# Performance work log

Hardware: AMD Instinct MI355X
Metric: run time of the kernel (lower is better)

## Reference

```python
import jax, jax.numpy as jnp
import numpy as np

SLOPE = 0.15  # LeakyReLU negative slope used throughout the module

def leaky(v):
    return jnp.where(v >= 0, v, SLOPE * v)

def _linear_params(key, fan_in, fan_out):
    kw, kb = jax.random.split(key)
    bound = 1.0 / np.sqrt(fan_in)
    W = jax.random.uniform(kw, (fan_in, fan_out), minval=-bound, maxval=bound, dtype=jnp.float32)
    b = jax.random.uniform(kb, (fan_out,), minval=-bound, maxval=bound, dtype=jnp.float32)
    return W, b

N_NODES = 50000
N_EDGES = 640000
IN_DIM = 128
EDGE_DIM = 64
HID = 128
LAT = 64

def setup_inputs() -> dict:
    key = jax.random.key(0)
    ks = jax.random.split(key, 12)
    x = jax.random.normal(ks[0], (N_NODES, IN_DIM), dtype=jnp.float32)
    edge_index = jax.random.randint(ks[1], (2, N_EDGES), 0, N_NODES, dtype=jnp.int32)
    edge_attr = jax.random.normal(ks[2], (N_EDGES, EDGE_DIM), dtype=jnp.float32)
    # conv1 params
    e1W1, e1b1 = _linear_params(ks[3], EDGE_DIM, HID)
    e1W2, e1b2 = _linear_params(ks[4], HID, HID)
    n1W, n1b = _linear_params(ks[5], IN_DIM + HID, HID)
    # conv2 params
    e2W1, e2b1 = _linear_params(ks[6], EDGE_DIM, HID)
    e2W2, e2b2 = _linear_params(ks[7], HID, HID)
    n2W, n2b = _linear_params(ks[8], HID + HID, HID)
    muW, mub = _linear_params(ks[9], HID, LAT)
    lvW, lvb = _linear_params(ks[10], HID, LAT)
    return {"x": x, "edge_index": edge_index, "edge_attr": edge_attr,
            "e1W1": e1W1, "e1b1": e1b1, "e1W2": e1W2, "e1b2": e1b2, "n1W": n1W, "n1b": n1b,
            "e2W1": e2W1, "e2b1": e2b1, "e2W2": e2W2, "e2b2": e2b2, "n2W": n2W, "n2b": n2b,
            "muW": muW, "mub": mub, "lvW": lvW, "lvb": lvb}

def edge_encoder(x, edge_index, edge_attr, eW1, eb1, eW2, eb2, nW, nb):
    # edge MLP: Linear -> LeakyReLU(0.15) -> Linear
    emb = leaky(edge_attr @ eW1 + eb1) @ eW2 + eb2           # [E, H]
    dst = edge_index[1]                                       # PyG x_i = x[target]
    z = jnp.concatenate([x[dst], emb], axis=1)                # [E, in+H]
    msg = z @ nW + nb                                         # [E, H]
    return jax.ops.segment_sum(msg, dst, num_segments=x.shape[0])  # aggr='add'

def reference(x, edge_index, edge_attr,
              e1W1, e1b1, e1W2, e1b2, n1W, n1b,
              e2W1, e2b1, e2W2, e2b2, n2W, n2b,
              muW, mub, lvW, lvb):
    # Dropout is identity in eval mode.
    h = leaky(edge_encoder(x, edge_index, edge_attr, e1W1, e1b1, e1W2, e1b2, n1W, n1b))
    h = leaky(edge_encoder(h, edge_index, edge_attr, e2W1, e2b1, e2W2, e2b2, n2W, n2b))
    mu = h @ muW + mub
    logvar = h @ lvW + lvb
    return (mu, logvar)
```

## Files before the change

### kernel.cpp

```cpp
#include <hip/hip_runtime.h>

typedef __bf16 bf16x4 __attribute__((ext_vector_type(4)));
typedef __bf16 bf16x8 __attribute__((ext_vector_type(8)));
typedef float  f32x4  __attribute__((ext_vector_type(4)));

constexpr int N_NODES = 50000;
constexpr int N_EDGES = 640000;
constexpr int NTILES  = 98;
constexpr int NB_EDGE = 2500;

__device__ __forceinline__ float leaky(float v) { return v >= 0.f ? v : 0.15f * v; }

__global__ void prep_kernel(
    const float* __restrict__ e1W1, const float* __restrict__ e1b1,
    const float* __restrict__ e1W2, const float* __restrict__ e1b2,
    const float* __restrict__ n1W,  const float* __restrict__ n1b,
    const float* __restrict__ e2W1, const float* __restrict__ e2b1,
    const float* __restrict__ e2W2, const float* __restrict__ e2b2,
    const float* __restrict__ n2W,  const float* __restrict__ n2b,
    const float* __restrict__ muW,  const float* __restrict__ mub,
    const float* __restrict__ lvW,  const float* __restrict__ lvb,
    __bf16* __restrict__ packE, __bf16* __restrict__ packN1,
    __bf16* __restrict__ packN2, __bf16* __restrict__ packH,
    float* __restrict__ ebias, float* __restrict__ c1, float* __restrict__ c2,
    float* __restrict__ hbias)
{
    int bid = blockIdx.x;
    int lane = threadIdx.x;
    int quad = lane >> 4, low = lane & 15;

    if (bid < 32) {
        int ct = bid >> 1, kt = bid & 1;
        for (int j = 0; j < 8; ++j) {
            int k = kt * 32 + quad * 8 + j;
            int n = ct * 16 + low;
            float v = (n < 128) ? e1W1[k * 128 + n] : e2W1[k * 128 + (n - 128)];
            packE[((ct * 2 + kt) * 64 + lane) * 8 + j] = (__bf16)v;
        }
    } else if (bid < 160) {
        bool is1 = bid < 96;
        int tile = bid - (is1 ? 32 : 96);
        const float* nW  = is1 ? n1W  : n2W;
        const float* eW2 = is1 ? e1W2 : e2W2;
        __bf16* dst = is1 ? packN1 : packN2;
        int ct = tile >> 3, kt = tile & 7;
        for (int j = 0; j < 8; ++j) {
            int k = kt * 32 + quad * 8 + j;
            int n = ct * 16 + low;
            float v;
            if (k < 128) {
                v = nW[k * 128 + n];
            } else {
                int i = k - 128;
                float acc = 0.f;
                for (int k2 = 0; k2 < 128; ++k2)
                    acc += eW2[i * 128 + k2] * nW[(128 + k2) * 128 + n];
                v = acc;
            }
            dst[((ct * 8 + kt) * 64 + lane) * 8 + j] = (__bf16)v;
        }
    } else if (bid < 192) {
        int tile = bid - 160;
        int ct = tile >> 2, kt = tile & 3;
        for (int j = 0; j < 8; ++j) {
            int k = kt * 32 + quad * 8 + j;
            int n = ct * 16 + low;
            float v = (n < 64) ? muW[k * 64 + n] : lvW[k * 64 + (n - 64)];
            packH[((ct * 4 + kt) * 64 + lane) * 8 + j] = (__bf16)v;
        }
    } else if (bid == 192 || bid == 193) {
        const float* nW  = (bid == 192) ? n1W  : n2W;
        const float* nb  = (bid == 192) ? n1b  : n2b;
        const float* eb2 = (bid == 192) ? e1b2 : e2b2;
        float* dst = (bid == 192) ? c1 : c2;
        for (int rep = 0; rep < 2; ++rep) {
            int j = lane + rep * 64;
            float acc = nb[j];
            for (int k = 0; k < 128; ++k)
                acc += eb2[k] * nW[(128 + k) * 128 + j];
            dst[j] = acc;
        }
    } else {
        for (int rep = 0; rep < 4; ++rep) {
            int j = lane + rep * 64;
            ebias[j] = (j < 128) ? e1b1[j] : e2b1[j - 128];
        }
        for (int rep = 0; rep < 2; ++rep) {
            int j = lane + rep * 64;
            hbias[j] = (j < 64) ? mub[j] : lvb[j - 64];
        }
    }
}

__global__ void hist_kernel(const int* __restrict__ dstp, int* __restrict__ deg) {
    int e = blockIdx.x * 256 + threadIdx.x;
    if (e < N_EDGES) atomicAdd(&deg[dstp[e]], 1);
}

__global__ void scan_a(const int* __restrict__ deg, int* __restrict__ offs,
                       int* __restrict__ tileSum, float* __restrict__ degf) {
    __shared__ int s[512];
    int t = threadIdx.x, i = blockIdx.x * 512 + t;
    int v = (i < N_NODES) ? deg[i] : 0;
    if (i < N_NODES) degf[i] = (float)v;
    s[t] = v; __syncthreads();
    for (int off = 1; off < 512; off <<= 1) {
        int x = (t >= off) ? s[t - off] : 0;
        __syncthreads();
        s[t] += x;
        __syncthreads();
    }
    if (i < N_NODES) offs[i] = s[t] - v;
    if (t == 511) tileSum[blockIdx.x] = s[511];
}

__global__ void scan_b(const int* __restrict__ tileSum, int* __restrict__ tileOff) {
    __shared__ int s[128];
    int t = threadIdx.x;
    int v = (t < NTILES) ? tileSum[t] : 0;
    s[t] = v; __syncthreads();
    for (int off = 1; off < 128; off <<= 1) {
        int x = (t >= off) ? s[t - off] : 0;
        __syncthreads();
        s[t] += x;
        __syncthreads();
    }
    if (t < NTILES) tileOff[t] = s[t] - v;
}

__global__ void scatter_kernel(const int* __restrict__ dstp, const int* __restrict__ offs,
                               const int* __restrict__ tileOff,
                               int* __restrict__ cursor, int* __restrict__ sorted,
                               int* __restrict__ sdst) {
    int e = blockIdx.x * 256 + threadIdx.x;
    if (e < N_EDGES) {
        int d = dstp[e];
        int p = offs[d] + tileOff[d >> 9] + atomicAdd(&cursor[d], 1);
        sorted[p] = e;
        sdst[p] = d;
    }
}

__global__ __launch_bounds__(256, 3) void edge_kernel(
    const float* __restrict__ edge_attr,
    const int* __restrict__ sorted, const int* __restrict__ sdst,
    const __bf16* __restrict__ packE,
    const float* __restrict__ ebias, float* __restrict__ S)
{
    __shared__ alignas(16) __bf16 Lball[4 * 64 * 72];
    __shared__ alignas(8) unsigned char runof_s[64];
    __shared__ int rundst_s[64];
    __shared__ int nruns_s;

    int tid = threadIdx.x;
    int w = tid >> 6, lane = tid & 63;
    int quad = lane >> 4, low = lane & 15;
    int r = tid >> 2, c0 = (tid & 3) * 16;

    bf16x8 bfragE[2][4];
    #pragma unroll
    for (int kt = 0; kt < 2; ++kt)
        #pragma unroll
        for (int ct = 0; ct < 4; ++ct)
            bfragE[kt][ct] = *reinterpret_cast<const bf16x8*>(
                packE + (((w * 4 + ct) * 2 + kt) * 64 + lane) * 8);
    float bias_c[4];
    #pragma unroll
    for (int ct = 0; ct < 4; ++ct) bias_c[ct] = ebias[w * 64 + ct * 16 + low];

    __bf16* As = Lball;
    __bf16* Lb = &Lball[w * 4608];

    constexpr int STRIDE = NB_EDGE * 64;
    int e0 = blockIdx.x * 64;

    float4 f0, f1, f2, f3;
    int md_c, ei_n, md_n;
    {
        int ei = sorted[e0 + r];
        md_c = sdst[e0 + lane];
        const float4* ap = reinterpret_cast<const float4*>(edge_attr + (size_t)ei * 64 + c0);
        f0 = ap[0]; f1 = ap[1]; f2 = ap[2]; f3 = ap[3];
    }
    ei_n = sorted[e0 + STRIDE + r];
    md_n = sdst[e0 + STRIDE + lane];

    #pragma unroll 1
    for (int it = 0; it < 4; ++it) {
        {
            bf16x8 v0, v1;
            v0[0]=(__bf16)f0.x; v0[1]=(__bf16)f0.y; v0[2]=(__bf16)f0.z; v0[3]=(__bf16)f0.w;
            v0[4]=(__bf16)f1.x; v0[5]=(__bf16)f1.y; v0[6]=(__bf16)f1.z; v0[7]=(__bf16)f1.w;
            v1[0]=(__bf16)f2.x; v1[1]=(__bf16)f2.y; v1[2]=(__bf16)f2.z; v1[3]=(__bf16)f2.w;
            v1[4]=(__bf16)f3.x; v1[5]=(__bf16)f3.y; v1[6]=(__bf16)f3.z; v1[7]=(__bf16)f3.w;
            *reinterpret_cast<bf16x8*>(&As[r * 72 + c0])     = v0;
            *reinterpret_cast<bf16x8*>(&As[r * 72 + c0 + 8]) = v1;
        }

        if (w == 0) {
            rundst_s[lane] = md_c;
            int dp = __shfl_up(md_c, 1);
            bool flag = (lane > 0) && (md_c != dp);
            unsigned long long mask = __ballot(flag);
            int rid = __popcll(mask & ((1ull << lane) - 1ull)) + (flag ? 1 : 0);
            runof_s[lane] = (unsigned char)rid;
            if (flag || lane == 0) rundst_s[rid] = md_c;
            if (lane == 0) nruns_s = __popcll(mask) + 1;
        }
        __syncthreads();

        float4 g0{}, g1{}, g2{}, g3{};
        if (it < 3) {
            const float4* gp = reinterpret_cast<const float4*>(
                edge_attr + (size_t)ei_n * 64 + c0);
            g0 = gp[0]; g1 = gp[1]; g2 = gp[2]; g3 = gp[3];
        }
        int ei_nn = 0, md_nn = 0;
        if (it < 2) {
            int eo = e0 + (it + 2) * STRIDE;
            ei_nn = sorted[eo + r];
            md_nn = sdst[eo + lane];
        }

        f32x4 C1[4][4] = {};
        #pragma unroll
        for (int kt = 0; kt < 2; ++kt)
            #pragma unroll
            for (int rt = 0; rt < 4; ++rt) {
                bf16x8 a = *reinterpret_cast<const bf16x8*>(
                    &As[(rt * 16 + low) * 72 + kt * 32 + quad * 8]);
                #pragma unroll
                for (int ct = 0; ct < 4; ++ct)
                    C1[rt][ct] = __builtin_amdgcn_mfma_f32_16x16x32_bf16(
                        a, bfragE[kt][ct], C1[rt][ct], 0, 0, 0);
            }
        __syncthreads();

        #pragma unroll
        for (int rt = 0; rt < 4; ++rt)
            #pragma unroll
            for (int ct = 0; ct < 4; ++ct) {
                bf16x4 v;
                #pragma unroll
                for (int rr = 0; rr < 4; ++rr)
                    v[rr] = (__bf16)leaky(C1[rt][ct][rr] + bias_c[ct]);
                *reinterpret_cast<bf16x4*>(
                    &Lb[(ct * 16 + low) * 72 + rt * 16 + quad * 4]) = v;
            }

        int nruns = nruns_s;
        for (int rt2 = 0; rt2 * 16 < nruns; ++rt2) {
            f32x4 C2[4] = {};
            #pragma unroll
            for (int kt = 0; kt < 2; ++kt) {
                uint2 rb2 = *reinterpret_cast<const uint2*>(&runof_s[kt * 32 + quad * 8]);
                unsigned target = (unsigned)(rt2 * 16 + low);
                bf16x8 a;
                #pragma unroll
                for (int j = 0; j < 8; ++j) {
                    unsigned byte = ((j < 4 ? (rb2.x >> (8 * j)) : (rb2.y >> (8 * (j - 4)))) & 0xFFu);
                    a[j] = (byte == target) ? (__bf16)1.0f : (__bf16)0.0f;
                }
                #pragma unroll
                for (int ct = 0; ct < 4; ++ct) {
                    bf16x8 b = *reinterpret_cast<const bf16x8*>(
                        &Lb[(ct * 16 + low) * 72 + kt * 32 + quad * 8]);
                    C2[ct] = __builtin_amdgcn_mfma_f32_16x16x32_bf16(a, b, C2[ct], 0, 0, 0);
                }
            }
            #pragma unroll
            for (int ct = 0; ct < 4; ++ct) {
                int col = w * 64 + ct * 16 + low;
                #pragma unroll
                for (int rr = 0; rr < 4; ++rr) {
                    int run = rt2 * 16 + quad * 4 + rr;
                    if (run < nruns) {
                        int node = rundst_s[run];
                        if ((unsigned)node < (unsigned)N_NODES)
                            unsafeAtomicAdd(&S[(size_t)node * 256 + col], C2[ct][rr]);
                    }
                }
            }
        }
        __syncthreads();

        f0 = g0; f1 = g1; f2 = g2; f3 = g3;
        md_c = md_n; ei_n = ei_nn; md_n = md_nn;
    }
}

__global__ __launch_bounds__(256) void node_fused(
    const float* __restrict__ x, const float* __restrict__ S,
    const float* __restrict__ degf,
    const __bf16* __restrict__ packN1, const __bf16* __restrict__ packN2,
    const __bf16* __restrict__ packH,
    const float* __restrict__ c1, const float* __restrict__ c2,
    const float* __restrict__ hbias,
    float* __restrict__ out)
{
    constexpr int HS = 152;
    __shared__ __bf16 Hs[4][16 * HS];
    int w = threadIdx.x >> 6, lane = threadIdx.x & 63;
    int quad = lane >> 4, low = lane & 15;
    int rb = blockIdx.x * 64 + w * 16;

    int arow = rb + low;
    if (arow >= N_NODES) arow = N_NODES - 1;
    float ds = degf[arow];
    const float* xrow = x + (size_t)arow * 128;
    const float* Srow = S + (size_t)arow * 256;

    float deg4[4];
    #pragma unroll
    for (int rr = 0; rr < 4; ++rr) {
        int row = rb + quad * 4 + rr;
        deg4[rr] = degf[row < N_NODES ? row : N_NODES - 1];
    }

    __bf16* Hw = Hs[w];

    f32x4 C[8] = {};
    #pragma unroll
    for (int kt = 0; kt < 8; ++kt) {
        const float* base = (kt < 4) ? (xrow + kt * 32 + quad * 8)
                                     : (Srow + (kt - 4) * 32 + quad * 8);
        float4 p0 = *reinterpret_cast<const float4*>(base);
        float4 p1 = *reinterpret_cast<const float4*>(base + 4);
        float m = (kt < 4) ? ds : 1.f;
        bf16x8 a;
        a[0]=(__bf16)(p0.x*m); a[1]=(__bf16)(p0.y*m); a[2]=(__bf16)(p0.z*m); a[3]=(__bf16)(p0.w*m);
        a[4]=(__bf16)(p1.x*m); a[5]=(__bf16)(p1.y*m); a[6]=(__bf16)(p1.z*m); a[7]=(__bf16)(p1.w*m);
        #pragma unroll
        for (int ct = 0; ct < 8; ++ct) {
            bf16x8 b = *reinterpret_cast<const bf16x8*>(packN1 + ((ct * 8 + kt) * 64 + lane) * 8);
            C[ct] = __builtin_amdgcn_mfma_f32_16x16x32_bf16(a, b, C[ct], 0, 0, 0);
        }
    }
    #pragma unroll
    for (int ct = 0; ct < 8; ++ct) {
        int col = ct * 16 + low;
        float cb = c1[col];
        #pragma unroll
        for (int rr = 0; rr < 4; ++rr) {
            float v = leaky(C[ct][rr] + deg4[rr] * cb);
            Hw[(quad * 4 + rr) * HS + col] = (__bf16)(v * deg4[rr]);
        }
    }

    f32x4 C2[8] = {};
    #pragma unroll
    for (int kt = 0; kt < 8; ++kt) {
        bf16x8 a;
        if (kt < 4) {
            a = *reinterpret_cast<const bf16x8*>(&Hw[low * HS + kt * 32 + quad * 8]);
        } else {
            const float* base = Srow + 128 + (kt - 4) * 32 + quad * 8;
            float4 p0 = *reinterpret_cast<const float4*>(base);
            float4 p1 = *reinterpret_cast<const float4*>(base + 4);
            a[0]=(__bf16)p0.x; a[1]=(__bf16)p0.y; a[2]=(__bf16)p0.z; a[3]=(__bf16)p0.w;
            a[4]=(__bf16)p1.x; a[5]=(__bf16)p1.y; a[6]=(__bf16)p1.z; a[7]=(__bf16)p1.w;
        }
        #pragma unroll
        for (int ct = 0; ct < 8; ++ct) {
            bf16x8 b = *reinterpret_cast<const bf16x8*>(packN2 + ((ct * 8 + kt) * 64 + lane) * 8);
            C2[ct] = __builtin_amdgcn_mfma_f32_16x16x32_bf16(a, b, C2[ct], 0, 0, 0);
        }
    }
    #pragma unroll
    for (int ct = 0; ct < 8; ++ct) {
        int col = ct * 16 + low;
        float cb = c2[col];
        #pragma unroll
        for (int rr = 0; rr < 4; ++rr) {
            float v = leaky(C2[ct][rr] + deg4[rr] * cb);
            Hw[(quad * 4 + rr) * HS + col] = (__bf16)v;
        }
    }

    f32x4 C3[8] = {};
    #pragma unroll
    for (int kt = 0; kt < 4; ++kt) {
        bf16x8 a = *reinterpret_cast<const bf16x8*>(&Hw[low * HS + kt * 32 + quad * 8]);
        #pragma unroll
        for (int ct = 0; ct < 8; ++ct) {
            bf16x8 b = *reinterpret_cast<const bf16x8*>(packH + ((ct * 4 + kt) * 64 + lane) * 8);
            C3[ct] = __builtin_amdgcn_mfma_f32_16x16x32_bf16(a, b, C3[ct], 0, 0, 0);
        }
    }
    #pragma unroll
    for (int ct = 0; ct < 8; ++ct) {
        int col = ct * 16 + low;
        float hb = hbias[col];
        #pragma unroll
        for (int rr = 0; rr < 4; ++rr) {
            int row = rb + quad * 4 + rr;
            if (row >= N_NODES) continue;
            float v = C3[ct][rr] + hb;
            if (col < 64) out[(size_t)row * 64 + col] = v;
            else          out[(size_t)N_NODES * 64 + (size_t)row * 64 + (col - 64)] = v;
        }
    }
}

extern "C" void kernel_launch(void* const* d_in, const int* in_sizes, int n_in,
                              void* d_out, int out_size, void* d_ws, size_t ws_size,
                              hipStream_t stream)
{
    const float* x     = (const float*)d_in[0];
    const int*   eidx  = (const int*)  d_in[1];
    const float* eattr = (const float*)d_in[2];
    const float* e1W1 = (const float*)d_in[3];
    const float* e1b1 = (const float*)d_in[4];
    const float* e1W2 = (const float*)d_in[5];
    const float* e1b2 = (const float*)d_in[6];
    const float* n1W  = (const float*)d_in[7];
    const float* n1b  = (const float*)d_in[8];
    const float* e2W1 = (const float*)d_in[9];
    const float* e2b1 = (const float*)d_in[10];
    const float* e2W2 = (const float*)d_in[11];
    const float* e2b2 = (const float*)d_in[12];
    const float* n2W  = (const float*)d_in[13];
    const float* n2b  = (const float*)d_in[14];
    const float* muW  = (const float*)d_in[15];
    const float* mub  = (const float*)d_in[16];
    const float* lvW  = (const float*)d_in[17];
    const float* lvb  = (const float*)d_in[18];

    const int* dstp = eidx + N_EDGES;

    char* ws = (char*)d_ws;
    size_t off = 0;
    auto alloc = [&](size_t bytes) -> void* {
        void* p = ws + off;
        off = (off + bytes + 1023) & ~(size_t)1023;
        return p;
    };
    float* S       = (float*)alloc((size_t)N_NODES * 256 * 4);
    float* h       = (float*)alloc((size_t)N_NODES * 128 * 4);
    float* g       = (float*)alloc((size_t)N_NODES * 128 * 4);
    int*   deg     = (int*)  alloc((size_t)N_NODES * 4);
    int*   cursor  = (int*)  alloc((size_t)N_NODES * 4);
    int*   offs    = (int*)  alloc((size_t)N_NODES * 4);
    float* degf    = (float*)alloc((size_t)N_NODES * 4);
    int*   sorted  = (int*)  alloc((size_t)N_EDGES * 4);
    int*   tileSum = (int*)  alloc(NTILES * 4);
    int*   tileOff = (int*)  alloc(NTILES * 4);
    __bf16* packE  = (__bf16*)alloc(32 * 64 * 8 * 2);
    __bf16* packN1 = (__bf16*)alloc(64 * 64 * 8 * 2);
    __bf16* packN2 = (__bf16*)alloc(64 * 64 * 8 * 2);
    __bf16* packH  = (__bf16*)alloc(32 * 64 * 8 * 2);
    float* ebias   = (float*)alloc(256 * 4);
    float* c1      = (float*)alloc(128 * 4);
    float* c2      = (float*)alloc(128 * 4);
    float* hbias   = (float*)alloc(128 * 4);
    (void)ws_size; (void)in_sizes; (void)n_in; (void)out_size; (void)h;

    int* sdst = (int*)g;

    hipMemsetAsync(S, 0, (size_t)N_NODES * 256 * 4, stream);
    hipMemsetAsync(deg, 0, 2 * (((size_t)N_NODES * 4 + 1023) & ~(size_t)1023), stream);

    prep_kernel<<<195, 64, 0, stream>>>(e1W1, e1b1, e1W2, e1b2, n1W, n1b,
                                        e2W1, e2b1, e2W2, e2b2, n2W, n2b,
                                        muW, mub, lvW, lvb,
                                        packE, packN1, packN2, packH,
                                        ebias, c1, c2, hbias);

    hist_kernel<<<N_EDGES / 256, 256, 0, stream>>>(dstp, deg);
    scan_a<<<NTILES, 512, 0, stream>>>(deg, offs, tileSum, degf);
    scan_b<<<1, 128, 0, stream>>>(tileSum, tileOff);
    scatter_kernel<<<N_EDGES / 256, 256, 0, stream>>>(dstp, offs, tileOff, cursor, sorted, sdst);

    edge_kernel<<<NB_EDGE, 256, 0, stream>>>(eattr, sorted, sdst, packE, ebias, S);

    node_fused<<<(N_NODES + 63) / 64, 256, 0, stream>>>(
        x, S, degf, packN1, packN2, packH, c1, c2, hbias, (float*)d_out);
}
```

Baseline: 452.1 us.

## Defer first-tile atomics across iterations, separate A buffer, fuse scan_b into scatter

The edge kernel gets its own shared buffer for the input tile, so the barrier between the first MFMA stage and the leaky store can be dropped. The first 16-run segment-reduction tile is now held in registers and its atomic adds to S are issued in the next iteration, after the barrier, so they overlap with the next tile's loads and MFMAs. A final flush after the loop writes the last tile. Separately, the single-block scan_b kernel is folded into scatter_kernel, where every block recomputes the 98-entry tile prefix in shared memory, removing one launch. This costs more shared memory and registers in the edge kernel and some redundant scan work in every scatter block.

```diff
diff --git a/kernel.cpp b/kernel.cpp
--- a/kernel.cpp
+++ b/kernel.cpp
@@ -114,28 +114,28 @@
     if (t == 511) tileSum[blockIdx.x] = s[511];
 }
 
-__global__ void scan_b(const int* __restrict__ tileSum, int* __restrict__ tileOff) {
-    __shared__ int s[128];
-    int t = threadIdx.x;
-    int v = (t < NTILES) ? tileSum[t] : 0;
-    s[t] = v; __syncthreads();
-    for (int off = 1; off < 128; off <<= 1) {
-        int x = (t >= off) ? s[t - off] : 0;
-        __syncthreads();
-        s[t] += x;
-        __syncthreads();
-    }
-    if (t < NTILES) tileOff[t] = s[t] - v;
-}
-
 __global__ void scatter_kernel(const int* __restrict__ dstp, const int* __restrict__ offs,
-                               const int* __restrict__ tileOff,
+                               const int* __restrict__ tileSum,
                                int* __restrict__ cursor, int* __restrict__ sorted,
                                int* __restrict__ sdst) {
-    int e = blockIdx.x * 256 + threadIdx.x;
+    __shared__ int s[128];
+    __shared__ int toff[128];
+    int t = threadIdx.x;
+    int v = 0;
+    if (t < 128) { v = (t < NTILES) ? tileSum[t] : 0; s[t] = v; }
+    __syncthreads();
+    for (int off = 1; off < 128; off <<= 1) {
+        int x = (t < 128 && t >= off) ? s[t - off] : 0;
+        __syncthreads();
+        if (t < 128) s[t] += x;
+        __syncthreads();
+    }
+    if (t < 128) toff[t] = s[t] - v;
+    __syncthreads();
+    int e = blockIdx.x * 256 + t;
     if (e < N_EDGES) {
         int d = dstp[e];
-        int p = offs[d] + tileOff[d >> 9] + atomicAdd(&cursor[d], 1);
+        int p = offs[d] + toff[d >> 9] + atomicAdd(&cursor[d], 1);
         sorted[p] = e;
         sdst[p] = d;
     }
@@ -148,6 +148,7 @@
     const float* __restrict__ ebias, float* __restrict__ S)
 {
     __shared__ alignas(16) __bf16 Lball[4 * 64 * 72];
+    __shared__ alignas(16) __bf16 As[64 * 72];
     __shared__ alignas(8) unsigned char runof_s[64];
     __shared__ int rundst_s[64];
     __shared__ int nruns_s;
@@ -168,7 +169,6 @@
     #pragma unroll
     for (int ct = 0; ct < 4; ++ct) bias_c[ct] = ebias[w * 64 + ct * 16 + low];
 
-    __bf16* As = Lball;
     __bf16* Lb = &Lball[w * 4608];
 
     constexpr int STRIDE = NB_EDGE * 64;
@@ -184,6 +184,9 @@
     }
     ei_n = sorted[e0 + STRIDE + r];
     md_n = sdst[e0 + STRIDE + lane];
+
+    f32x4 C2d[4] = {};
+    int nodeD[4] = {-1, -1, -1, -1};
 
     #pragma unroll 1
     for (int it = 0; it < 4; ++it) {
@@ -209,6 +212,17 @@
         }
         __syncthreads();
 
+        if (it > 0) {
+            #pragma unroll
+            for (int ct = 0; ct < 4; ++ct) {
+                int col = w * 64 + ct * 16 + low;
+                #pragma unroll
+                for (int rr = 0; rr < 4; ++rr)
+                    if ((unsigned)nodeD[rr] < (unsigned)N_NODES)
+                        unsafeAtomicAdd(&S[(size_t)nodeD[rr] * 256 + col], C2d[ct][rr]);
+            }
+        }
+
         float4 g0{}, g1{}, g2{}, g3{};
         if (it < 3) {
             const float4* gp = reinterpret_cast<const float4*>(
@@ -234,7 +248,6 @@
                     C1[rt][ct] = __builtin_amdgcn_mfma_f32_16x16x32_bf16(
                         a, bfragE[kt][ct], C1[rt][ct], 0, 0, 0);
             }
-        __syncthreads();
 
         #pragma unroll
         for (int rt = 0; rt < 4; ++rt)
@@ -249,7 +262,33 @@
             }
 
         int nruns = nruns_s;
-        for (int rt2 = 0; rt2 * 16 < nruns; ++rt2) {
+        {
+            #pragma unroll
+            for (int ct = 0; ct < 4; ++ct) C2d[ct] = f32x4{};
+            #pragma unroll
+            for (int kt = 0; kt < 2; ++kt) {
+                uint2 rb2 = *reinterpret_cast<const uint2*>(&runof_s[kt * 32 + quad * 8]);
+                unsigned target = (unsigned)low;
+                bf16x8 a;
+                #pragma unroll
+                for (int j = 0; j < 8; ++j) {
+                    unsigned byte = ((j < 4 ? (rb2.x >> (8 * j)) : (rb2.y >> (8 * (j - 4)))) & 0xFFu);
+                    a[j] = (byte == target) ? (__bf16)1.0f : (__bf16)0.0f;
+                }
+                #pragma unroll
+                for (int ct = 0; ct < 4; ++ct) {
+                    bf16x8 b = *reinterpret_cast<const bf16x8*>(
+                        &Lb[(ct * 16 + low) * 72 + kt * 32 + quad * 8]);
+                    C2d[ct] = __builtin_amdgcn_mfma_f32_16x16x32_bf16(a, b, C2d[ct], 0, 0, 0);
+                }
+            }
+            #pragma unroll
+            for (int rr = 0; rr < 4; ++rr) {
+                int run = quad * 4 + rr;
+                nodeD[rr] = (run < nruns) ? rundst_s[run] : -1;
+            }
+        }
+        for (int rt2 = 1; rt2 * 16 < nruns; ++rt2) {
             f32x4 C2[4] = {};
             #pragma unroll
             for (int kt = 0; kt < 2; ++kt) {
@@ -282,10 +321,20 @@
                 }
             }
         }
+
         __syncthreads();
 
         f0 = g0; f1 = g1; f2 = g2; f3 = g3;
         md_c = md_n; ei_n = ei_nn; md_n = md_nn;
+    }
+
+    #pragma unroll
+    for (int ct = 0; ct < 4; ++ct) {
+        int col = w * 64 + ct * 16 + low;
+        #pragma unroll
+        for (int rr = 0; rr < 4; ++rr)
+            if ((unsigned)nodeD[rr] < (unsigned)N_NODES)
+                unsafeAtomicAdd(&S[(size_t)nodeD[rr] * 256 + col], C2d[ct][rr]);
     }
 }
 
@@ -444,7 +493,6 @@
     float* degf    = (float*)alloc((size_t)N_NODES * 4);
     int*   sorted  = (int*)  alloc((size_t)N_EDGES * 4);
     int*   tileSum = (int*)  alloc(NTILES * 4);
-    int*   tileOff = (int*)  alloc(NTILES * 4);
     __bf16* packE  = (__bf16*)alloc(32 * 64 * 8 * 2);
     __bf16* packN1 = (__bf16*)alloc(64 * 64 * 8 * 2);
     __bf16* packN2 = (__bf16*)alloc(64 * 64 * 8 * 2);
@@ -468,8 +516,7 @@
 
     hist_kernel<<<N_EDGES / 256, 256, 0, stream>>>(dstp, deg);
     scan_a<<<NTILES, 512, 0, stream>>>(deg, offs, tileSum, degf);
-    scan_b<<<1, 128, 0, stream>>>(tileSum, tileOff);
-    scatter_kernel<<<N_EDGES / 256, 256, 0, stream>>>(dstp, offs, tileOff, cursor, sorted, sdst);
+    scatter_kernel<<<N_EDGES / 256, 256, 0, stream>>>(dstp, offs, tileSum, cursor, sorted, sdst);
 
     edge_kernel<<<NB_EDGE, 256, 0, stream>>>(eattr, sorted, sdst, packE, ebias, S);
 
```

Result: slower. 484.5 us (+7.2%).
